# Optimization experiments

Hardware: AMD Instinct MI355X
Metric: run time of the kernel (lower is better)

## Reference

```python
import jax, jax.numpy as jnp
import numpy as np

B, C, H, W = 2, 3, 512, 512
P = 16
D = 768
NH = 12
DEPTH = 12
MLP = 4
HP, WP = H // P, W // P
N = HP * WP
DH = D // NH          # 64
ROPE_BASE = 100.0     # from pos_embed='RoPE100'


def _ln(x, w, b, eps):
    m = jnp.mean(x, -1, keepdims=True)
    v = jnp.mean((x - m) ** 2, -1, keepdims=True)
    return (x - m) * jax.lax.rsqrt(v + eps) * w + b


def _rope_tables(maxpos, d):
    inv = 1.0 / (ROPE_BASE ** (jnp.arange(0, d, 2, dtype=jnp.float32) / d))
    f = jnp.arange(maxpos, dtype=jnp.float32)[:, None] * inv[None, :]
    f = jnp.concatenate([f, f], -1)  # [maxpos, d]
    return jnp.cos(f), jnp.sin(f)


def _rot_half(x):
    x1, x2 = jnp.split(x, 2, -1)
    return jnp.concatenate([-x2, x1], -1)


def _rope2d(t, pos, cos, sin):
    # t: [B,NH,N,DH]; pos: [B,N,2] (y,x). First half of DH rotated by y, second by x.
    def rot1d(tok, p):
        c = cos[p][:, None]  # [B,1,N,DH//2]
        s = sin[p][:, None]
        return tok * c + _rot_half(tok) * s
    ty, tx = jnp.split(t, 2, -1)
    return jnp.concatenate([rot1d(ty, pos[..., 0]), rot1d(tx, pos[..., 1])], -1)


def _forward(image, patch_w, patch_b, ln1_w, ln1_b, qkv_w, qkv_b, proj_w, proj_b,
             ln2_w, ln2_b, fc1_w, fc1_b, fc2_w, fc2_b, encn_w, encn_b):
    # patch embed: conv stride=patch, flatten row-major (y-major, matching cartesian_prod(y,x))
    x = jax.lax.conv_general_dilated(image, patch_w, (P, P), 'VALID',
                                     dimension_numbers=('NCHW', 'OIHW', 'NCHW'))
    x = (x + patch_b[None, :, None, None]).reshape(B, D, N).transpose(0, 2, 1)  # [B,N,D]
    yy, xx = jnp.meshgrid(jnp.arange(HP), jnp.arange(WP), indexing='ij')
    pos = jnp.broadcast_to(jnp.stack([yy, xx], -1).reshape(N, 2), (B, N, 2))
    cos, sin = _rope_tables(max(HP, WP), DH // 2)
    scale = DH ** -0.5
    for i in range(DEPTH):
        h = _ln(x, ln1_w[i], ln1_b[i], 1e-5)
        qkv = (h @ qkv_w[i].T + qkv_b[i]).reshape(B, N, 3, NH, DH).transpose(2, 0, 3, 1, 4)
        q, k, v = qkv[0], qkv[1], qkv[2]  # [B,NH,N,DH]
        q = _rope2d(q, pos, cos, sin)
        k = _rope2d(k, pos, cos, sin)
        att = jax.nn.softmax(jnp.einsum('bhqd,bhkd->bhqk', q, k) * scale, -1)
        o = jnp.einsum('bhqk,bhkd->bhqd', att, v).transpose(0, 2, 1, 3).reshape(B, N, D)
        x = x + o @ proj_w[i].T + proj_b[i]
        h = _ln(x, ln2_w[i], ln2_b[i], 1e-5)
        h = jax.nn.gelu(h @ fc1_w[i].T + fc1_b[i], approximate=False)
        x = x + h @ fc2_w[i].T + fc2_b[i]
    x = _ln(x, encn_w, encn_b, 1e-6)
    return x, pos


def setup_inputs() -> dict:
    key = jax.random.key(0)
    ks = jax.random.split(key, 8)
    s = 0.02
    dff = MLP * D
    return {
        "image": jax.random.normal(ks[0], (B, C, H, W), jnp.float32),
        "true_shape": jnp.full((B, 2), H, jnp.int32),
        "patch_w": jax.random.normal(ks[1], (D, C, P, P), jnp.float32) * s,
        "patch_b": jnp.zeros((D,), jnp.float32),
        "ln1_w": jnp.ones((DEPTH, D), jnp.float32),
        "ln1_b": jnp.zeros((DEPTH, D), jnp.float32),
        "qkv_w": jax.random.normal(ks[2], (DEPTH, 3 * D, D), jnp.float32) * s,
        "qkv_b": jnp.zeros((DEPTH, 3 * D), jnp.float32),
        "proj_w": jax.random.normal(ks[3], (DEPTH, D, D), jnp.float32) * s,
        "proj_b": jnp.zeros((DEPTH, D), jnp.float32),
        "ln2_w": jnp.ones((DEPTH, D), jnp.float32),
        "ln2_b": jnp.zeros((DEPTH, D), jnp.float32),
        "fc1_w": jax.random.normal(ks[4], (DEPTH, dff, D), jnp.float32) * s,
        "fc1_b": jnp.zeros((DEPTH, dff), jnp.float32),
        "fc2_w": jax.random.normal(ks[5], (DEPTH, D, dff), jnp.float32) * s,
        "fc2_b": jnp.zeros((DEPTH, D), jnp.float32),
        "encn_w": jnp.ones((D,), jnp.float32),
        "encn_b": jnp.zeros((D,), jnp.float32),
    }


def reference(image, true_shape, patch_w, patch_b, ln1_w, ln1_b, qkv_w, qkv_b,
              proj_w, proj_b, ln2_w, ln2_b, fc1_w, fc1_b, fc2_w, fc2_b,
              encn_w, encn_b):
    # true_shape assumed full-resolution (all images H x W); positions are static grid
    return _forward(image, patch_w, patch_b, ln1_w, ln1_b, qkv_w, qkv_b, proj_w,
                    proj_b, ln2_w, ln2_b, fc1_w, fc1_b, fc2_w, fc2_b, encn_w, encn_b)
```

## Files before the change

### kernel.cpp

```cpp
#include <hip/hip_runtime.h>
#include <hip/hip_bf16.h>
#include <stdint.h>

typedef unsigned short u16;
typedef __attribute__((ext_vector_type(8))) short bf16x8;
typedef __attribute__((ext_vector_type(4))) float f32x4;
typedef __attribute__((ext_vector_type(4))) u16 u16x4;

__device__ __forceinline__ u16 f2bf(float f) {
  union { float f; uint32_t u; } v; v.f = f;
  uint32_t u = v.u + 0x7FFFu + ((v.u >> 16) & 1u);
  return (u16)(u >> 16);
}
__device__ __forceinline__ float bf2f(u16 h) {
  union { uint32_t u; float f; } v; v.u = ((uint32_t)h) << 16;
  return v.f;
}

__device__ __forceinline__ int xcd_swz(int hw, int n) {
  return (n & 7) ? hw : (hw & 7) * (n >> 3) + (hw >> 3);
}

__device__ __forceinline__ void gload_lds16(const void* g, void* l) {
  __builtin_amdgcn_global_load_lds(
      (const __attribute__((address_space(1))) void*)g,
      (__attribute__((address_space(3))) void*)l, 16, 0, 0);
}

__global__ __launch_bounds__(256) void cast_f32_bf16(const float* __restrict__ src,
                                                     u16* __restrict__ dst, int n4) {
  int i = blockIdx.x * 256 + threadIdx.x;
  if (i < n4) {
    float4 v = ((const float4*)src)[i];
    u16x4 o; o.x = f2bf(v.x); o.y = f2bf(v.y); o.z = f2bf(v.z); o.w = f2bf(v.w);
    ((u16x4*)dst)[i] = o;
  }
}

__global__ __launch_bounds__(256) void im2col_kernel(const float* __restrict__ img,
                                                     u16* __restrict__ out) {
  int f = blockIdx.x * 256 + threadIdx.x;
  int row = blockIdx.y;
  int b = row >> 10, n = row & 1023, py = n >> 5, px = n & 31;
  int c = f >> 8, rem = f & 255, i = rem >> 4, j = rem & 15;
  float v = img[(((size_t)b * 3 + c) * 512 + py * 16 + i) * 512 + px * 16 + j];
  out[(size_t)row * 768 + f] = f2bf(v);
}

template <int EPI>
__global__ __launch_bounds__(256, 2)
void gemm_bt(const u16* __restrict__ A, const u16* __restrict__ W,
             const float* __restrict__ bias, void* __restrict__ outp,
             int M, int N, int K, int lda, int ldw) {
  constexpr int AB = 128 * 128;
  constexpr int BB = 128 * 128;
  constexpr int BUF = AB + BB;
  constexpr int LOADS = BUF / 4096;
  __shared__ char smem[2 * BUF];
  const int tid = threadIdx.x;
  const int lane = tid & 63;
  const int w = tid >> 6;
  const int qr = lane & 15;
  const int kg = lane >> 4;
  const int gx = gridDim.x;
  const int lid = xcd_swz(blockIdx.x + blockIdx.y * gx, gx * gridDim.y);
  const int bn = lid % gx, bm = lid / gx;
  const int wr = (w >> 1) * 64;
  const int wc = (w & 1) * 64;
  const size_t arow0 = (size_t)bm * 128;
  const size_t wrow0 = (size_t)bn * 128;
  const u16* Ab = A + (size_t)blockIdx.z * K;
  const u16* Wb = W + (size_t)blockIdx.z * K;

  f32x4 acc[4][4] = {};

  auto stage = [&](int buf, int kt) {
    char* As = smem + buf * BUF;
    char* Ws = As + AB;
#pragma unroll
    for (int r = 0; r < 4; ++r) {
      int o = r * 4096 + tid * 16;
      int row = o >> 7;
      int lc = (o & 127) ^ ((row & 7) << 4);
      gload_lds16(Ab + (arow0 + row) * lda + kt + (lc >> 1), As + o);
    }
#pragma unroll
    for (int r = 0; r < 4; ++r) {
      int o = r * 4096 + tid * 16;
      int row = o >> 7;
      int lc = (o & 127) ^ ((row & 7) << 4);
      gload_lds16(Wb + (wrow0 + row) * ldw + kt + (lc >> 1), Ws + o);
    }
  };

  const int nt = K >> 6;
  stage(0, 0);
  stage(1, 64);
  for (int t = 0; t < nt; ++t) {
    if (t + 1 < nt) {
      asm volatile("s_waitcnt vmcnt(%0)" :: "i"(LOADS) : "memory");
    } else {
      asm volatile("s_waitcnt vmcnt(0)" ::: "memory");
    }
    __builtin_amdgcn_s_barrier();
    const char* As = smem + (t & 1) * BUF;
    const char* Ws = As + AB;
    bf16x8 af[2][4], bfr[2][4];
#pragma unroll
    for (int ks = 0; ks < 2; ++ks) {
#pragma unroll
      for (int m = 0; m < 4; ++m) {
        int row = wr + m * 16 + qr;
        af[ks][m] = *(const bf16x8*)(As + row * 128 + ((ks * 64 + kg * 16) ^ ((row & 7) << 4)));
      }
#pragma unroll
      for (int n = 0; n < 4; ++n) {
        int row = wc + n * 16 + qr;
        bfr[ks][n] = *(const bf16x8*)(Ws + row * 128 + ((ks * 64 + kg * 16) ^ ((row & 7) << 4)));
      }
    }
    asm volatile("s_waitcnt lgkmcnt(0)" ::: "memory");
    __builtin_amdgcn_s_barrier();
    if (t + 2 < nt) stage(t & 1, (t + 2) << 6);
#pragma unroll
    for (int ks = 0; ks < 2; ++ks)
#pragma unroll
      for (int m = 0; m < 4; ++m)
#pragma unroll
        for (int n = 0; n < 4; ++n)
          acc[m][n] = __builtin_amdgcn_mfma_f32_16x16x32_bf16(af[ks][m], bfr[ks][n], acc[m][n], 0, 0, 0);
  }

  const int r0 = bm * 128 + wr + kg * 4;
  const int c0 = bn * 128 + wc + qr;
  if constexpr (EPI == 4) {
    const int headbase = bn * 128 + wc;
    const bool isqk = headbase < 1536;
    const float linv = exp2f(-0.41524101186092122f * (float)qr);
    u16* outb = (u16*)outp;
#pragma unroll
    for (int m = 0; m < 4; ++m) {
#pragma unroll
      for (int j = 0; j < 4; ++j) {
        int row = r0 + m * 16 + j;
        int tok = row & 1023;
        float vs[4];
#pragma unroll
        for (int n = 0; n < 4; ++n) vs[n] = acc[m][n][j] + bias[c0 + n * 16];
        if (isqk) {
          float sy, cy, sx, cx;
          __sincosf((float)(tok >> 5) * linv, &sy, &cy);
          __sincosf((float)(tok & 31) * linv, &sx, &cx);
          float a0 = vs[0], a1 = vs[1], a2 = vs[2], a3 = vs[3];
          vs[0] = a0 * cy - a1 * sy;
          vs[1] = a1 * cy + a0 * sy;
          vs[2] = a2 * cx - a3 * sx;
          vs[3] = a3 * cx + a2 * sx;
        }
#pragma unroll
        for (int n = 0; n < 4; ++n)
          outb[(size_t)row * N + c0 + n * 16] = f2bf(vs[n]);
      }
    }
  } else if constexpr (EPI == 5) {
    u16* outb = (u16*)outp + (size_t)blockIdx.z * M * N;
#pragma unroll
    for (int m = 0; m < 4; ++m)
#pragma unroll
      for (int j = 0; j < 4; ++j) {
        int row = r0 + m * 16 + j;
#pragma unroll
        for (int n = 0; n < 4; ++n)
          outb[(size_t)row * N + c0 + n * 16] = f2bf(acc[m][n][j]);
      }
  } else {
    u16* outb = (u16*)outp;
#pragma unroll
    for (int m = 0; m < 4; ++m)
#pragma unroll
      for (int j = 0; j < 4; ++j) {
        int row = r0 + m * 16 + j;
#pragma unroll
        for (int n = 0; n < 4; ++n) {
          int col = c0 + n * 16;
          float v = acc[m][n][j] + bias[col];
          v = 0.5f * v * (1.0f + erff(v * 0.70710678118654752f));
          outb[(size_t)row * N + col] = f2bf(v);
        }
      }
  }
}

template <int FINAL>
__global__ __launch_bounds__(256)
void fuse_red_ln(const u16* __restrict__ parts, const float* __restrict__ bias,
                 const float* __restrict__ resid, float* __restrict__ xout,
                 void* __restrict__ lnout, const float* __restrict__ lw,
                 const float* __restrict__ lb, float eps) {
  if (FINAL && blockIdx.x >= 2048) {
    int i = (blockIdx.x - 2048) * 256 + threadIdx.x;
    if (i < 4096) {
      int c = i & 1, n = (i >> 1) & 1023;
      ((float*)lnout)[(size_t)2048 * 768 + i] = (float)(c ? (n & 31) : (n >> 5));
    }
    return;
  }
  const int row = blockIdx.x, t = threadIdx.x;
  constexpr size_t MN = (size_t)2048 * 768;
  const u16* p0 = parts + (size_t)row * 768;
  float v[3];
#pragma unroll
  for (int e = 0; e < 3; ++e) {
    int c = t + e * 256;
    float s = bf2f(p0[c]) + bf2f(p0[MN + c]) + bf2f(p0[2 * MN + c]) + bf2f(p0[3 * MN + c]) + bias[c];
    if (resid) s += resid[(size_t)row * 768 + c];
    v[e] = s;
    xout[(size_t)row * 768 + c] = s;
  }
  float s = v[0] + v[1] + v[2];
  float sq = v[0] * v[0] + v[1] * v[1] + v[2] * v[2];
#pragma unroll
  for (int m = 1; m < 64; m <<= 1) {
    s += __shfl_xor(s, m);
    sq += __shfl_xor(sq, m);
  }
  __shared__ float red[8];
  int wv = t >> 6;
  if ((t & 63) == 0) { red[wv] = s; red[4 + wv] = sq; }
  __syncthreads();
  s = red[0] + red[1] + red[2] + red[3];
  sq = red[4] + red[5] + red[6] + red[7];
  float mean = s * (1.0f / 768.0f);
  float var = sq * (1.0f / 768.0f) - mean * mean;
  float rstd = rsqrtf(var + eps);
#pragma unroll
  for (int e = 0; e < 3; ++e) {
    int c = t + e * 256;
    float val = (v[e] - mean) * rstd * lw[c] + lb[c];
    if (FINAL)
      ((float*)lnout)[(size_t)row * 768 + c] = val;
    else
      ((u16*)lnout)[(size_t)row * 768 + c] = f2bf(val);
  }
}

__global__ __launch_bounds__(256)
void attn_kernel(const u16* __restrict__ qkv, u16* __restrict__ o) {
  __shared__ char smem[40960];
  const int tid = threadIdx.x, lane = tid & 63, w = tid >> 6;
  const int qr = lane & 15, kg = lane >> 4;
  const int lid = xcd_swz(blockIdx.x, gridDim.x);
  const int qb = lid & 15, bh = lid >> 4;
  const int b = bh / 12, h = bh % 12;
  const int qrow0 = qb * 64 + w * 16;
  const u16* kvb = qkv + (size_t)b * 1024 * 2304;

  bf16x8 aq[2];
  {
    const u16* qbase = qkv + ((size_t)(b * 1024 + qrow0 + qr)) * 2304 + h * 64;
    aq[0] = *(const bf16x8*)(qbase + kg * 8);
    aq[1] = *(const bf16x8*)(qbase + 32 + kg * 8);
#pragma unroll
    for (int r = 0; r < 2; ++r)
#pragma unroll
      for (int e = 0; e < 8; ++e)
        aq[r][e] = (short)f2bf(bf2f((u16)aq[r][e]) * 0.125f);
  }
  f32x4 oacc[4] = {};
  float lrun[4] = {0.f, 0.f, 0.f, 0.f};

  const int kvp = tid >> 3, dg = tid & 7;
  bf16x8 va, vb;
  auto issueV = [&](int kt) {
    const u16* vsrc = kvb + ((size_t)(kt * 64 + kvp * 2)) * 2304 + 1536 + h * 64 + dg * 8;
    va = *(const bf16x8*)vsrc;
    vb = *(const bf16x8*)(vsrc + 2304);
  };
  auto issueK = [&](int kt, int bsel) {
    char* Ks = smem + bsel * 8192;
#pragma unroll
    for (int r = 0; r < 2; ++r) {
      int off = r * 4096 + tid * 16;
      int kv = off >> 7;
      int db = (off ^ ((kv & 7) << 4)) & 127;
      gload_lds16(kvb + ((size_t)(kt * 64 + kv)) * 2304 + 768 + h * 64 + (db >> 1), Ks + off);
    }
  };
  auto writeV = [&](int bsel) {
    char* Vt = smem + 16384 + bsel * 8192;
#pragma unroll
    for (int j = 0; j < 8; ++j) {
      int d = dg * 8 + j;
      uint32_t pk = (uint32_t)(u16)va[j] | ((uint32_t)(u16)vb[j] << 16);
      *(uint32_t*)(Vt + ((d * 128 + kvp * 4) ^ (((dg ^ j) & 7) << 4))) = pk;
    }
  };

  issueV(0);
  issueK(0, 0);
  writeV(0);

  for (int kt = 0; kt < 16; ++kt) {
    const int c = kt & 1;
    asm volatile("s_waitcnt vmcnt(0) lgkmcnt(0)" ::: "memory");
    __builtin_amdgcn_s_barrier();
    if (kt + 1 < 16) { issueV(kt + 1); issueK(kt + 1, c ^ 1); }

    const char* Ks = smem + c * 8192;
    const char* Vt = smem + 16384 + c * 8192;
    char* Ps = smem + 32768 + w * 2048;

    f32x4 sa[4] = {};
#pragma unroll
    for (int ks = 0; ks < 2; ++ks)
#pragma unroll
      for (int n = 0; n < 4; ++n) {
        int row = n * 16 + qr;
        bf16x8 bk = *(const bf16x8*)(Ks + ((row * 128 + ks * 64 + kg * 16) ^ ((row & 7) << 4)));
        sa[n] = __builtin_amdgcn_mfma_f32_16x16x32_bf16(aq[ks], bk, sa[n], 0, 0, 0);
      }

    float pv[4][4];
#pragma unroll
    for (int j = 0; j < 4; ++j) {
#pragma unroll
      for (int n = 0; n < 4; ++n) pv[n][j] = __expf(sa[n][j]);
      lrun[j] += (pv[0][j] + pv[1][j]) + (pv[2][j] + pv[3][j]);
    }

    if (kt + 1 < 16) writeV(c ^ 1);

#pragma unroll
    for (int n = 0; n < 4; ++n)
#pragma unroll
      for (int j = 0; j < 4; ++j) {
        int row = kg * 4 + j;
        *(u16*)(Ps + ((row * 128 + (n * 16 + qr) * 2) ^ ((row & 7) << 4))) = f2bf(pv[n][j]);
      }
    bf16x8 pf[2];
    pf[0] = *(const bf16x8*)(Ps + ((qr * 128 + kg * 16) ^ ((qr & 7) << 4)));
    pf[1] = *(const bf16x8*)(Ps + ((qr * 128 + 64 + kg * 16) ^ ((qr & 7) << 4)));
#pragma unroll
    for (int ks = 0; ks < 2; ++ks)
#pragma unroll
      for (int n = 0; n < 4; ++n) {
        int d = n * 16 + qr;
        bf16x8 vf = *(const bf16x8*)(Vt + ((d * 128 + ks * 64 + kg * 16) ^ ((((d >> 3) ^ (d & 7)) & 7) << 4)));
        oacc[n] = __builtin_amdgcn_mfma_f32_16x16x32_bf16(pf[ks], vf, oacc[n], 0, 0, 0);
      }
  }
#pragma unroll
  for (int j = 0; j < 4; ++j)
#pragma unroll
    for (int msk = 1; msk < 16; msk <<= 1) lrun[j] += __shfl_xor(lrun[j], msk);
#pragma unroll
  for (int n = 0; n < 4; ++n)
#pragma unroll
    for (int j = 0; j < 4; ++j) {
      int rowg = b * 1024 + qrow0 + kg * 4 + j;
      int colg = h * 64 + n * 16 + qr;
      o[(size_t)rowg * 768 + colg] = f2bf(oacc[n][j] / lrun[j]);
    }
}

extern "C" void kernel_launch(void* const* d_in, const int* in_sizes, int n_in,
                              void* d_out, int out_size, void* d_ws, size_t ws_size,
                              hipStream_t stream) {
  const float* image  = (const float*)d_in[0];
  const float* patch_w = (const float*)d_in[2];
  const float* patch_b = (const float*)d_in[3];
  const float* ln1_w = (const float*)d_in[4];
  const float* ln1_b = (const float*)d_in[5];
  const float* qkv_w = (const float*)d_in[6];
  const float* qkv_b = (const float*)d_in[7];
  const float* proj_w = (const float*)d_in[8];
  const float* proj_b = (const float*)d_in[9];
  const float* ln2_w = (const float*)d_in[10];
  const float* ln2_b = (const float*)d_in[11];
  const float* fc1_w = (const float*)d_in[12];
  const float* fc1_b = (const float*)d_in[13];
  const float* fc2_w = (const float*)d_in[14];
  const float* fc2_b = (const float*)d_in[15];
  const float* encn_w = (const float*)d_in[16];
  const float* encn_b = (const float*)d_in[17];

  char* ws = (char*)d_ws;
  size_t off = 0;
  auto alloc = [&](size_t bytes) {
    char* pr = ws + off;
    off += (bytes + 255) & ~(size_t)255;
    return pr;
  };

  float* x    = (float*)alloc((size_t)2048 * 768 * 4);
  u16* hbuf   = (u16*)alloc((size_t)2048 * 768 * 2);
  u16* qkvb   = (u16*)alloc((size_t)2048 * 2304 * 2);
  u16* obuf   = (u16*)alloc((size_t)2048 * 768 * 2);
  u16* h2     = (u16*)alloc((size_t)2048 * 3072 * 2);
  u16* wpb    = (u16*)alloc((size_t)768 * 768 * 2);
  u16* parts  = (u16*)alloc((size_t)4 * 2048 * 768 * 2);

  const size_t wq_n = (size_t)12 * 2304 * 768;
  const size_t wp_n = (size_t)12 * 768 * 768;
  const size_t w1_n = (size_t)12 * 3072 * 768;
  const size_t w2_n = (size_t)12 * 3072 * 768;
  bool upfront = (off + 2 * (wq_n + wp_n + w1_n + w2_n) + (1u << 20)) <= ws_size;

  u16 *wq, *wp, *w1, *w2;
  if (upfront) {
    wq = (u16*)alloc(wq_n * 2);
    wp = (u16*)alloc(wp_n * 2);
    w1 = (u16*)alloc(w1_n * 2);
    w2 = (u16*)alloc(w2_n * 2);
  } else {
    wq = (u16*)alloc((size_t)2304 * 768 * 2);
    wp = (u16*)alloc((size_t)768 * 768 * 2);
    w1 = (u16*)alloc((size_t)3072 * 768 * 2);
    w2 = (u16*)alloc((size_t)3072 * 768 * 2);
  }

  auto cast = [&](const float* s, u16* d, size_t n) {
    int n4 = (int)(n / 4);
    cast_f32_bf16<<<(n4 + 255) / 256, 256, 0, stream>>>(s, d, n4);
  };

  cast(patch_w, wpb, (size_t)768 * 768);
  if (upfront) {
    cast(qkv_w, wq, wq_n);
    cast(proj_w, wp, wp_n);
    cast(fc1_w, w1, w1_n);
    cast(fc2_w, w2, w2_n);
  }

  im2col_kernel<<<dim3(3, 2048), 256, 0, stream>>>(image, hbuf);
  gemm_bt<5><<<dim3(6, 16, 4), 256, 0, stream>>>(hbuf, wpb, nullptr, parts, 2048, 768, 192, 768, 768);
  fuse_red_ln<0><<<2048, 256, 0, stream>>>(parts, patch_b, nullptr, x, hbuf, ln1_w, ln1_b, 1e-5f);

  for (int L = 0; L < 12; ++L) {
    u16 *wqL, *wpL, *w1L, *w2L;
    if (upfront) {
      wqL = wq + (size_t)L * 2304 * 768;
      wpL = wp + (size_t)L * 768 * 768;
      w1L = w1 + (size_t)L * 3072 * 768;
      w2L = w2 + (size_t)L * 3072 * 768;
    } else {
      cast(qkv_w + (size_t)L * 2304 * 768, wq, (size_t)2304 * 768);
      cast(proj_w + (size_t)L * 768 * 768, wp, (size_t)768 * 768);
      cast(fc1_w + (size_t)L * 3072 * 768, w1, (size_t)3072 * 768);
      cast(fc2_w + (size_t)L * 768 * 3072, w2, (size_t)3072 * 768);
      wqL = wq; wpL = wp; w1L = w1; w2L = w2;
    }
    gemm_bt<4><<<dim3(18, 16), 256, 0, stream>>>(hbuf, wqL, qkv_b + L * 2304, qkvb, 2048, 2304, 768, 768, 768);
    attn_kernel<<<384, 256, 0, stream>>>(qkvb, obuf);
    gemm_bt<5><<<dim3(6, 16, 4), 256, 0, stream>>>(obuf, wpL, nullptr, parts, 2048, 768, 192, 768, 768);
    fuse_red_ln<0><<<2048, 256, 0, stream>>>(parts, proj_b + L * 768, x, x, hbuf,
                                             ln2_w + L * 768, ln2_b + L * 768, 1e-5f);
    gemm_bt<1><<<dim3(24, 16), 256, 0, stream>>>(hbuf, w1L, fc1_b + L * 3072, h2, 2048, 3072, 768, 768, 768);
    gemm_bt<5><<<dim3(6, 16, 4), 256, 0, stream>>>(h2, w2L, nullptr, parts, 2048, 768, 768, 3072, 3072);
    if (L < 11) {
      fuse_red_ln<0><<<2048, 256, 0, stream>>>(parts, fc2_b + L * 768, x, x, hbuf,
                                               ln1_w + (L + 1) * 768, ln1_b + (L + 1) * 768, 1e-5f);
    } else {
      fuse_red_ln<1><<<2064, 256, 0, stream>>>(parts, fc2_b + L * 768, x, x, (float*)d_out,
                                               encn_w, encn_b, 1e-6f);
    }
  }
}
```

Baseline: 1.344 ms.

## Keep attention probabilities in registers via transposed MFMA and lane permutes

Swaps the MFMA operand order so S^T is computed, which leaves each lane holding one query row. That lets P be packed to bf16 with v_cvt_pk_bf16_f32 and redistributed using permlane32_swap and shuffles, instead of a round trip through LDS. This drops the per-wave P scratch buffer (LDS goes from 40 KB to 32 KB), simplifies the row-sum reduction, and vectorizes the output stores. It also adds s_setprio around the MFMA blocks. The risk is extra VALU and cross-lane work, plus fragile lane-mapping correctness.

```diff
diff --git a/kernel.cpp b/kernel.cpp
--- a/kernel.cpp
+++ b/kernel.cpp
@@ -6,6 +6,7 @@
 typedef __attribute__((ext_vector_type(8))) short bf16x8;
 typedef __attribute__((ext_vector_type(4))) float f32x4;
 typedef __attribute__((ext_vector_type(4))) u16 u16x4;
+typedef __attribute__((ext_vector_type(4))) uint32_t u32x4;
 
 __device__ __forceinline__ u16 f2bf(float f) {
   union { float f; uint32_t u; } v; v.f = f;
@@ -246,9 +247,10 @@
 
 __global__ __launch_bounds__(256)
 void attn_kernel(const u16* __restrict__ qkv, u16* __restrict__ o) {
-  __shared__ char smem[40960];
+  __shared__ char smem[32768];
   const int tid = threadIdx.x, lane = tid & 63, w = tid >> 6;
   const int qr = lane & 15, kg = lane >> 4;
+  const bool kgodd = (kg & 1) != 0;
   const int lid = xcd_swz(blockIdx.x, gridDim.x);
   const int qb = lid & 15, bh = lid >> 4;
   const int b = bh / 12, h = bh % 12;
@@ -267,7 +269,7 @@
         aq[r][e] = (short)f2bf(bf2f((u16)aq[r][e]) * 0.125f);
   }
   f32x4 oacc[4] = {};
-  float lrun[4] = {0.f, 0.f, 0.f, 0.f};
+  float lsum = 0.f;
 
   const int kvp = tid >> 3, dg = tid & 7;
   bf16x8 va, vb;
@@ -308,59 +310,80 @@
 
     const char* Ks = smem + c * 8192;
     const char* Vt = smem + 16384 + c * 8192;
-    char* Ps = smem + 32768 + w * 2048;
 
     f32x4 sa[4] = {};
+    __builtin_amdgcn_s_setprio(1);
 #pragma unroll
     for (int ks = 0; ks < 2; ++ks)
 #pragma unroll
       for (int n = 0; n < 4; ++n) {
         int row = n * 16 + qr;
         bf16x8 bk = *(const bf16x8*)(Ks + ((row * 128 + ks * 64 + kg * 16) ^ ((row & 7) << 4)));
-        sa[n] = __builtin_amdgcn_mfma_f32_16x16x32_bf16(aq[ks], bk, sa[n], 0, 0, 0);
-      }
+        sa[n] = __builtin_amdgcn_mfma_f32_16x16x32_bf16(bk, aq[ks], sa[n], 0, 0, 0);
+      }
+    __builtin_amdgcn_s_setprio(0);
 
     float pv[4][4];
-#pragma unroll
-    for (int j = 0; j < 4; ++j) {
-#pragma unroll
-      for (int n = 0; n < 4; ++n) pv[n][j] = __expf(sa[n][j]);
-      lrun[j] += (pv[0][j] + pv[1][j]) + (pv[2][j] + pv[3][j]);
-    }
+    float ts = 0.f;
+#pragma unroll
+    for (int n = 0; n < 4; ++n)
+#pragma unroll
+      for (int j = 0; j < 4; ++j) {
+        pv[n][j] = __expf(sa[n][j]);
+        ts += pv[n][j];
+      }
+    lsum += ts;
 
     if (kt + 1 < 16) writeV(c ^ 1);
 
-#pragma unroll
-    for (int n = 0; n < 4; ++n)
-#pragma unroll
-      for (int j = 0; j < 4; ++j) {
-        int row = kg * 4 + j;
-        *(u16*)(Ps + ((row * 128 + (n * 16 + qr) * 2) ^ ((row & 7) << 4))) = f2bf(pv[n][j]);
-      }
-    bf16x8 pf[2];
-    pf[0] = *(const bf16x8*)(Ps + ((qr * 128 + kg * 16) ^ ((qr & 7) << 4)));
-    pf[1] = *(const bf16x8*)(Ps + ((qr * 128 + 64 + kg * 16) ^ ((qr & 7) << 4)));
+    uint32_t pk0[4], pk1[4];
+#pragma unroll
+    for (int n = 0; n < 4; ++n) {
+      asm("v_cvt_pk_bf16_f32 %0, %1, %2" : "=v"(pk0[n]) : "v"(pv[n][0]), "v"(pv[n][1]));
+      asm("v_cvt_pk_bf16_f32 %0, %1, %2" : "=v"(pk1[n]) : "v"(pv[n][2]), "v"(pv[n][3]));
+    }
+
+    bf16x8 pb[2];
+#pragma unroll
+    for (int ks = 0; ks < 2; ++ks) {
+      uint32_t A0 = pk0[ks * 2], B0 = pk0[ks * 2 + 1];
+      uint32_t A1 = pk1[ks * 2], B1 = pk1[ks * 2 + 1];
+      asm("v_permlane32_swap_b32 %0, %1" : "+v"(A0), "+v"(B0));
+      asm("v_permlane32_swap_b32 %0, %1" : "+v"(A1), "+v"(B1));
+      uint32_t sA0 = (uint32_t)__shfl_xor((int)A0, 16);
+      uint32_t sA1 = (uint32_t)__shfl_xor((int)A1, 16);
+      uint32_t sB0 = (uint32_t)__shfl_xor((int)B0, 16);
+      uint32_t sB1 = (uint32_t)__shfl_xor((int)B1, 16);
+      u32x4 dd;
+      dd.x = kgodd ? sB0 : A0;
+      dd.y = kgodd ? sB1 : A1;
+      dd.z = kgodd ? B0 : sA0;
+      dd.w = kgodd ? B1 : sA1;
+      pb[ks] = __builtin_bit_cast(bf16x8, dd);
+    }
+
+    __builtin_amdgcn_s_setprio(1);
 #pragma unroll
     for (int ks = 0; ks < 2; ++ks)
 #pragma unroll
       for (int n = 0; n < 4; ++n) {
         int d = n * 16 + qr;
         bf16x8 vf = *(const bf16x8*)(Vt + ((d * 128 + ks * 64 + kg * 16) ^ ((((d >> 3) ^ (d & 7)) & 7) << 4)));
-        oacc[n] = __builtin_amdgcn_mfma_f32_16x16x32_bf16(pf[ks], vf, oacc[n], 0, 0, 0);
-      }
-  }
-#pragma unroll
-  for (int j = 0; j < 4; ++j)
-#pragma unroll
-    for (int msk = 1; msk < 16; msk <<= 1) lrun[j] += __shfl_xor(lrun[j], msk);
-#pragma unroll
-  for (int n = 0; n < 4; ++n)
-#pragma unroll
-    for (int j = 0; j < 4; ++j) {
-      int rowg = b * 1024 + qrow0 + kg * 4 + j;
-      int colg = h * 64 + n * 16 + qr;
-      o[(size_t)rowg * 768 + colg] = f2bf(oacc[n][j] / lrun[j]);
-    }
+        oacc[n] = __builtin_amdgcn_mfma_f32_16x16x32_bf16(vf, pb[ks], oacc[n], 0, 0, 0);
+      }
+    __builtin_amdgcn_s_setprio(0);
+  }
+  lsum += __shfl_xor(lsum, 16);
+  lsum += __shfl_xor(lsum, 32);
+  float inv = 1.0f / lsum;
+  const size_t rowg = (size_t)(b * 1024 + qrow0 + qr);
+#pragma unroll
+  for (int n = 0; n < 4; ++n) {
+    u16x4 ov;
+#pragma unroll
+    for (int j = 0; j < 4; ++j) ov[j] = f2bf(oacc[n][j] * inv);
+    *(u16x4*)(o + rowg * 768 + h * 64 + n * 16 + kg * 4) = ov;
+  }
 }
 
 extern "C" void kernel_launch(void* const* d_in, const int* in_sizes, int n_in,
```

Result: faster. 1.303 ms (-3.0%).
